# Performance work log

Hardware: AMD Instinct MI355X
Metric: run time of the kernel (lower is better)

The kernel has to match this reference:

```python
import jax, jax.numpy as jnp
import numpy as np

SCALES = (1, 3, 6)
PRECISION = 10  # pywt default: 2**10 samples of psi on [-5, 5]


def _gaus1_filters():
    """Replicates pywt.cwt's integrated-wavelet filters for wavelet='gaus1'.

    pywt: psi, x = wavelet.wavefun(10); int_psi = cumsum(psi)*step; per scale a:
    j = arange(a*(x[-1]-x[0])+1)/(a*step) -> int indices; filter = int_psi[j][::-1];
    conv = np.convolve(data, filter). np.convolve flips its kernel, so the
    equivalent cross-correlation kernel (lax.conv semantics) is int_psi[j].
    """
    x = np.linspace(-5.0, 5.0, 2 ** PRECISION)
    step = x[1] - x[0]
    psi = -2.0 * x * np.exp(-x ** 2) / (np.pi / 2.0) ** 0.25
    int_psi = np.cumsum(psi) * step
    filts = []
    for a in SCALES:
        j = (np.arange(a * (x[-1] - x[0]) + 1) / (a * step)).astype(np.int64)
        j = j[j < int_psi.size]
        filts.append(int_psi[j].astype(np.float32))  # correlation kernel
    return filts

_FILTS = _gaus1_filters()


def setup_inputs() -> dict:
    key = jax.random.key(0)
    x = jax.random.normal(key, (32, 4096, 64), dtype=jnp.float32)
    return {"x": x}


def reference(x):
    B, S, C = x.shape
    sig = jnp.transpose(x, (0, 2, 1)).reshape(B * C, 1, S)  # [B*C, 1, S]
    outs = []
    for a, f in zip(SCALES, _FILTS):
        L = f.shape[0]
        k = jnp.asarray(f).reshape(1, 1, L)
        # full convolution (np.convolve): pad L-1 both sides
        conv = jax.lax.conv_general_dilated(
            sig, k, window_strides=(1,), padding=[(L - 1, L - 1)],
            dimension_numbers=("NCH", "OIH", "NCH"))  # [B*C, 1, S+L-1]
        coef = -np.sqrt(a).astype(np.float32) * jnp.diff(conv, axis=-1)  # [B*C,1,S+L-2]
        d = (coef.shape[-1] - S) / 2.0
        coef = coef[..., int(np.floor(d)): coef.shape[-1] - int(np.ceil(d))]  # [B*C,1,S]
        outs.append(coef)
    out = jnp.concatenate(outs, axis=1).reshape(B, C, len(SCALES), S)
    return jnp.transpose(out, (0, 2, 3, 1))  # [B, 3, S, C]
```

## Files before the change

kernel.cpp:

```cpp
#include <hip/hip_runtime.h>
#include <math.h>

#define S_LEN  4096
#define NCH    64
#define TILE_S 64
#define NT     4
#define RPT    8
#define TY     8
#define NQR    48
#define NQS    49
#define WQ     18
#define PQ     5
#define WLEN   72

struct WtArgs { float w6[62]; float w3[32]; float w1[12]; };


template <int T, int R>
struct FmaR {
  static __device__ __forceinline__ void run(const WtArgs& W, const float (&win)[WLEN],
                                             float (&a6)[RPT], float (&a3)[RPT],
                                             float (&a1)[RPT]) {
    a6[R] = fmaf(W.w6[T], win[T + R + 1], a6[R]);
    if constexpr (T >= 15 && T <= 46) a3[R] = fmaf(W.w3[T - 15], win[T + R + 1], a3[R]);
    if constexpr (T >= 25 && T <= 36) a1[R] = fmaf(W.w1[T - 25], win[T + R + 1], a1[R]);
    FmaR<T, R + 1>::run(W, win, a6, a3, a1);
  }
};
template <int T>
struct FmaR<T, RPT> {
  static __device__ __forceinline__ void run(const WtArgs&, const float (&)[WLEN],
                                             float (&)[RPT], float (&)[RPT], float (&)[RPT]) {}
};

template <int Q>
static __device__ __forceinline__ void load_quad(const float* __restrict__ colbase, int Q0,
                                                 float (&win)[WLEN]) {
  int s = Q0 + Q; if (s >= NQR) s -= NQR;
  const float4 v = *(const float4*)(colbase + (s << 2));
  win[4 * Q + 0] = v.x; win[4 * Q + 1] = v.y; win[4 * Q + 2] = v.z; win[4 * Q + 3] = v.w;
}

template <int Q>
struct PreQ {
  static __device__ __forceinline__ void run(const float* __restrict__ colbase, int Q0,
                                             float (&win)[WLEN]) {
    load_quad<Q>(colbase, Q0, win);
    PreQ<Q + 1>::run(colbase, Q0, win);
  }
};
template <>
struct PreQ<PQ> {
  static __device__ __forceinline__ void run(const float* __restrict__, int, float (&)[WLEN]) {}
};

template <int T>
struct Step {
  static __device__ __forceinline__ void run(const float* __restrict__ colbase, int Q0,
                                             const WtArgs& W, float (&win)[WLEN],
                                             float (&a6)[RPT], float (&a3)[RPT],
                                             float (&a1)[RPT]) {
    if constexpr ((T % 4 == 0) && (T / 4 + PQ < WQ))
      load_quad<T / 4 + PQ>(colbase, Q0, win);
    FmaR<T, 0>::run(W, win, a6, a3, a1);
    Step<T + 1>::run(colbase, Q0, W, win, a6, a3, a1);
  }
};
template <>
struct Step<62> {
  static __device__ __forceinline__ void run(const float* __restrict__, int, const WtArgs&,
                                             float (&)[WLEN], float (&)[RPT],
                                             float (&)[RPT], float (&)[RPT]) {}
};

template <int R>
struct Store {
  static __device__ __forceinline__ void run(float* __restrict__ o1, float* __restrict__ o3,
                                             float* __restrict__ o6, const float (&a6)[RPT],
                                             const float (&a3)[RPT], const float (&a1)[RPT]) {
    o1[(size_t)R * NCH] = a1[R];
    o3[(size_t)R * NCH] = a3[R];
    o6[(size_t)R * NCH] = a6[R];
    Store<R + 1>::run(o1, o3, o6, a6, a3, a1);
  }
};
template <>
struct Store<RPT> {
  static __device__ __forceinline__ void run(float* __restrict__, float* __restrict__,
                                             float* __restrict__, const float (&)[RPT],
                                             const float (&)[RPT], const float (&)[RPT]) {}
};

template <int R>
struct Zero {
  static __device__ __forceinline__ void run(float (&a6)[RPT], float (&a3)[RPT], float (&a1)[RPT]) {
    a6[R] = 0.f; a3[R] = 0.f; a1[R] = 0.f;
    Zero<R + 1>::run(a6, a3, a1);
  }
};
template <>
struct Zero<RPT> {
  static __device__ __forceinline__ void run(float (&)[RPT], float (&)[RPT], float (&)[RPT]) {}
};

__global__ __launch_bounds__(512, 4)
void cwt_main(const float* __restrict__ x, float* __restrict__ out, const WtArgs W) {
  __shared__ __align__(16) float lds[NCH * NQS * 4];

  const int c  = threadIdx.x;
  const int ty = threadIdx.y;

  const int hw = blockIdx.x;
  const int wg = ((hw & 7) << 6) + (hw >> 3);
  const int gp = wg & 15;
  const int b  = wg >> 4;
  const int s0b = gp * (TILE_S * NT);
  const int ROW0 = s0b - 32;

  const float* __restrict__ xb = x + (size_t)b * S_LEN * NCH;
  const float* __restrict__ colbase = &lds[c * (NQS * 4)];

  {
    float pg[4][4];
    #pragma unroll
    for (int k = 0; k < 4; ++k) {
      const int g = 4 * ty + k;
      #pragma unroll
      for (int j = 0; j < 4; ++j) {
        const int row = ROW0 + 4 * g + j;
        float v = 0.f;
        if ((unsigned)row < (unsigned)S_LEN) v = xb[(size_t)row * NCH + c];
        pg[k][j] = v;
      }
    }
    #pragma unroll
    for (int k = 0; k < 4; ++k) {
      const int g = 4 * ty + k;
      *(float4*)&lds[c * (NQS * 4) + (g << 2)] =
          make_float4(pg[k][0], pg[k][1], pg[k][2], pg[k][3]);
    }
  }
  __syncthreads();

  #pragma clang loop unroll(disable)
  for (int i = 0; i < NT; ++i) {
    float sg[2][4];
    if (i < NT - 1) {
      #pragma unroll
      for (int k = 0; k < 2; ++k) {
        const int g = 32 + 16 * i + 2 * ty + k;
        #pragma unroll
        for (int j = 0; j < 4; ++j) {
          const int row = ROW0 + 4 * g + j;
          float v = 0.f;
          if ((unsigned)row < (unsigned)S_LEN) v = xb[(size_t)row * NCH + c];
          sg[k][j] = v;
        }
      }
    }

    float win[WLEN];
    float a6[RPT], a3[RPT], a1[RPT];
    Zero<0>::run(a6, a3, a1);
    const int Q0 = 16 * i + 2 * ty;
    PreQ<0>::run(colbase, Q0, win);
    Step<0>::run(colbase, Q0, W, win, a6, a3, a1);

    const int srow = s0b + TILE_S * i + RPT * ty;
    float* o1 = out + (((size_t)b * 3 + 0) * S_LEN + srow) * NCH + c;
    float* o3 = out + (((size_t)b * 3 + 1) * S_LEN + srow) * NCH + c;
    float* o6 = out + (((size_t)b * 3 + 2) * S_LEN + srow) * NCH + c;
    Store<0>::run(o1, o3, o6, a6, a3, a1);

    if (i < NT - 1) {
      #pragma unroll
      for (int k = 0; k < 2; ++k) {
        const int g = 32 + 16 * i + 2 * ty + k;
        const int s = (g < NQR) ? g : g - NQR;
        *(float4*)&lds[c * (NQS * 4) + (s << 2)] =
            make_float4(sg[k][0], sg[k][1], sg[k][2], sg[k][3]);
      }
    }
    __syncthreads();
  }
}

extern "C" void kernel_launch(void* const* d_in, const int* in_sizes, int n_in,
                              void* d_out, int out_size, void* d_ws, size_t ws_size,
                              hipStream_t stream) {
  (void)n_in; (void)out_size; (void)d_ws; (void)ws_size;
  const float* x = (const float*)d_in[0];
  float* out = (float*)d_out;
  const int B = in_sizes[0] / (S_LEN * NCH);

  WtArgs W;
  {
    static double ip[1024];
    const double delta = 10.0 / 1023.0;
    const double step  = (-5.0 + delta) + 5.0;
    const double cn    = pow(3.141592653589793 * 0.5, 0.25);
    double s = 0.0;
    for (int i = 0; i < 1024; ++i) {
      const double xi  = (i == 1023) ? 5.0 : ((double)i * delta - 5.0);
      const double psi = (-2.0 * xi) * exp(-(xi * xi)) / cn;
      s += psi;
      ip[i] = s * step;
    }
    const int   as_[3] = {6, 3, 1};
    const int   lf_[3] = {61, 31, 11};
    float*      wp_[3] = {W.w6, W.w3, W.w1};
    for (int si = 0; si < 3; ++si) {
      const double denom = (double)as_[si] * step;
      const float  sqa   = (float)sqrt((double)as_[si]);
      const int    lf    = lf_[si];
      for (int t = 0; t <= lf; ++t) {
        float km1 = 0.f, kt = 0.f;
        if (t >= 1)      km1 = (float)ip[(long)(((double)(t - 1)) / denom)];
        if (t <= lf - 1) kt  = (float)ip[(long)(((double)t) / denom)];
        wp_[si][t] = -sqa * (km1 - kt);
      }
    }
  }

  const int nblk = (S_LEN / (TILE_S * NT)) * B;
  dim3 grid(nblk);
  dim3 block(NCH, TY);
  hipLaunchKernelGGL(cwt_main, grid, block, 0, stream, x, out, W);
}
```

Measured before the change: 137.9 us.

## Bake filter weights as constexpr immediates and use one tile per block

```diff
diff --git a/kernel.cpp b/kernel.cpp
--- a/kernel.cpp
+++ b/kernel.cpp
@@ -4,49 +4,97 @@
 #define S_LEN  4096
 #define NCH    64
 #define TILE_S 64
-#define NT     4
 #define RPT    8
 #define TY     8
-#define NQR    48
-#define NQS    49
+#define NQ     32
+#define NQS    33
 #define WQ     18
 #define PQ     5
 #define WLEN   72
 
-struct WtArgs { float w6[62]; float w3[32]; float w1[12]; };
-
+
+constexpr double cexp_(double v) {
+  const double LN2 = 0.6931471805599453;
+  double t = v / LN2;
+  int k = (int)t;
+  if (t < 0.0 && (double)k != t) --k;
+  double r = v - (double)k * LN2;
+  double term = 1.0, sum = 1.0;
+  for (int n = 1; n <= 22; ++n) { term *= r / (double)n; sum += term; }
+  while (k > 0) { sum *= 2.0; --k; }
+  while (k < 0) { sum *= 0.5; ++k; }
+  return sum;
+}
+constexpr double csqrt_(double a) {
+  double y = a > 1.0 ? a : 1.0;
+  for (int i = 0; i < 64; ++i) y = 0.5 * (y + a / y);
+  return y;
+}
+struct Wt { float w6[62]; float w3[32]; float w1[12]; };
+constexpr Wt make_weights() {
+  Wt w{};
+  double ip[1024] = {};
+  const double delta = 10.0 / 1023.0;
+  const double step  = (-5.0 + delta) + 5.0;
+  const double cn    = csqrt_(csqrt_(1.5707963267948966));
+  double s = 0.0;
+  for (int i = 0; i < 1024; ++i) {
+    const double xi  = (i == 1023) ? 5.0 : ((double)i * delta - 5.0);
+    const double psi = (-2.0 * xi) * cexp_(-(xi * xi)) / cn;
+    s += psi;
+    ip[i] = s * step;
+  }
+  const int as_[3] = {6, 3, 1};
+  const int lf_[3] = {61, 31, 11};
+  for (int si = 0; si < 3; ++si) {
+    const double denom = (double)as_[si] * step;
+    const float  sqa   = (float)csqrt_((double)as_[si]);
+    const int    lf    = lf_[si];
+    for (int t = 0; t <= lf; ++t) {
+      float km1 = 0.f, kt = 0.f;
+      if (t >= 1)      km1 = (float)ip[(long)(((double)(t - 1)) / denom)];
+      if (t <= lf - 1) kt  = (float)ip[(long)(((double)t) / denom)];
+      const float val = -sqa * (km1 - kt);
+      if (si == 0) w.w6[t] = val; else if (si == 1) w.w3[t] = val; else w.w1[t] = val;
+    }
+  }
+  return w;
+}
+constexpr Wt CW = make_weights();
+template <int T> constexpr float W6 = CW.w6[T];
+template <int T> constexpr float W3 = CW.w3[T];
+template <int T> constexpr float W1 = CW.w1[T];
 
 template <int T, int R>
 struct FmaR {
-  static __device__ __forceinline__ void run(const WtArgs& W, const float (&win)[WLEN],
+  static __device__ __forceinline__ void run(const float (&win)[WLEN],
                                              float (&a6)[RPT], float (&a3)[RPT],
                                              float (&a1)[RPT]) {
-    a6[R] = fmaf(W.w6[T], win[T + R + 1], a6[R]);
-    if constexpr (T >= 15 && T <= 46) a3[R] = fmaf(W.w3[T - 15], win[T + R + 1], a3[R]);
-    if constexpr (T >= 25 && T <= 36) a1[R] = fmaf(W.w1[T - 25], win[T + R + 1], a1[R]);
-    FmaR<T, R + 1>::run(W, win, a6, a3, a1);
+    a6[R] = fmaf(W6<T>, win[T + R + 1], a6[R]);
+    if constexpr (T >= 15 && T <= 46) a3[R] = fmaf(W3<T - 15>, win[T + R + 1], a3[R]);
+    if constexpr (T >= 25 && T <= 36) a1[R] = fmaf(W1<T - 25>, win[T + R + 1], a1[R]);
+    FmaR<T, R + 1>::run(win, a6, a3, a1);
   }
 };
 template <int T>
 struct FmaR<T, RPT> {
-  static __device__ __forceinline__ void run(const WtArgs&, const float (&)[WLEN],
+  static __device__ __forceinline__ void run(const float (&)[WLEN],
                                              float (&)[RPT], float (&)[RPT], float (&)[RPT]) {}
 };
 
 template <int Q>
-static __device__ __forceinline__ void load_quad(const float* __restrict__ colbase, int Q0,
+static __device__ __forceinline__ void load_quad(const float* __restrict__ colbase, int q0,
                                                  float (&win)[WLEN]) {
-  int s = Q0 + Q; if (s >= NQR) s -= NQR;
-  const float4 v = *(const float4*)(colbase + (s << 2));
+  const float4 v = *(const float4*)(colbase + ((q0 + Q) << 2));
   win[4 * Q + 0] = v.x; win[4 * Q + 1] = v.y; win[4 * Q + 2] = v.z; win[4 * Q + 3] = v.w;
 }
 
 template <int Q>
 struct PreQ {
-  static __device__ __forceinline__ void run(const float* __restrict__ colbase, int Q0,
+  static __device__ __forceinline__ void run(const float* __restrict__ colbase, int q0,
                                              float (&win)[WLEN]) {
-    load_quad<Q>(colbase, Q0, win);
-    PreQ<Q + 1>::run(colbase, Q0, win);
+    load_quad<Q>(colbase, q0, win);
+    PreQ<Q + 1>::run(colbase, q0, win);
   }
 };
 template <>
@@ -56,21 +104,19 @@
 
 template <int T>
 struct Step {
-  static __device__ __forceinline__ void run(const float* __restrict__ colbase, int Q0,
-                                             const WtArgs& W, float (&win)[WLEN],
-                                             float (&a6)[RPT], float (&a3)[RPT],
-                                             float (&a1)[RPT]) {
+  static __device__ __forceinline__ void run(const float* __restrict__ colbase, int q0,
+                                             float (&win)[WLEN], float (&a6)[RPT],
+                                             float (&a3)[RPT], float (&a1)[RPT]) {
     if constexpr ((T % 4 == 0) && (T / 4 + PQ < WQ))
-      load_quad<T / 4 + PQ>(colbase, Q0, win);
-    FmaR<T, 0>::run(W, win, a6, a3, a1);
-    Step<T + 1>::run(colbase, Q0, W, win, a6, a3, a1);
+      load_quad<T / 4 + PQ>(colbase, q0, win);
+    FmaR<T, 0>::run(win, a6, a3, a1);
+    Step<T + 1>::run(colbase, q0, win, a6, a3, a1);
   }
 };
 template <>
 struct Step<62> {
-  static __device__ __forceinline__ void run(const float* __restrict__, int, const WtArgs&,
-                                             float (&)[WLEN], float (&)[RPT],
-                                             float (&)[RPT], float (&)[RPT]) {}
+  static __device__ __forceinline__ void run(const float* __restrict__, int, float (&)[WLEN],
+                                             float (&)[RPT], float (&)[RPT], float (&)[RPT]) {}
 };
 
 template <int R>
@@ -103,31 +149,29 @@
   static __device__ __forceinline__ void run(float (&)[RPT], float (&)[RPT], float (&)[RPT]) {}
 };
 
-__global__ __launch_bounds__(512, 4)
-void cwt_main(const float* __restrict__ x, float* __restrict__ out, const WtArgs W) {
+__global__ __launch_bounds__(512, 6)
+void cwt_main(const float* __restrict__ x, float* __restrict__ out) {
   __shared__ __align__(16) float lds[NCH * NQS * 4];
 
   const int c  = threadIdx.x;
   const int ty = threadIdx.y;
 
   const int hw = blockIdx.x;
-  const int wg = ((hw & 7) << 6) + (hw >> 3);
-  const int gp = wg & 15;
-  const int b  = wg >> 4;
-  const int s0b = gp * (TILE_S * NT);
-  const int ROW0 = s0b - 32;
+  const int wg = ((hw & 7) << 8) + (hw >> 3);
+  const int sx = wg & 63;
+  const int b  = wg >> 6;
+  const int s0 = sx * TILE_S;
+  const int ROW0 = s0 - 32;
 
   const float* __restrict__ xb = x + (size_t)b * S_LEN * NCH;
-  const float* __restrict__ colbase = &lds[c * (NQS * 4)];
 
   {
     float pg[4][4];
     #pragma unroll
     for (int k = 0; k < 4; ++k) {
-      const int g = 4 * ty + k;
       #pragma unroll
       for (int j = 0; j < 4; ++j) {
-        const int row = ROW0 + 4 * g + j;
+        const int row = ROW0 + 16 * ty + 4 * k + j;
         float v = 0.f;
         if ((unsigned)row < (unsigned)S_LEN) v = xb[(size_t)row * NCH + c];
         pg[k][j] = v;
@@ -135,54 +179,27 @@
     }
     #pragma unroll
     for (int k = 0; k < 4; ++k) {
-      const int g = 4 * ty + k;
-      *(float4*)&lds[c * (NQS * 4) + (g << 2)] =
+      const int q = 4 * ty + k;
+      *(float4*)&lds[c * (NQS * 4) + (q << 2)] =
           make_float4(pg[k][0], pg[k][1], pg[k][2], pg[k][3]);
     }
   }
   __syncthreads();
 
-  #pragma clang loop unroll(disable)
-  for (int i = 0; i < NT; ++i) {
-    float sg[2][4];
-    if (i < NT - 1) {
-      #pragma unroll
-      for (int k = 0; k < 2; ++k) {
-        const int g = 32 + 16 * i + 2 * ty + k;
-        #pragma unroll
-        for (int j = 0; j < 4; ++j) {
-          const int row = ROW0 + 4 * g + j;
-          float v = 0.f;
-          if ((unsigned)row < (unsigned)S_LEN) v = xb[(size_t)row * NCH + c];
-          sg[k][j] = v;
-        }
-      }
-    }
-
-    float win[WLEN];
-    float a6[RPT], a3[RPT], a1[RPT];
-    Zero<0>::run(a6, a3, a1);
-    const int Q0 = 16 * i + 2 * ty;
-    PreQ<0>::run(colbase, Q0, win);
-    Step<0>::run(colbase, Q0, W, win, a6, a3, a1);
-
-    const int srow = s0b + TILE_S * i + RPT * ty;
-    float* o1 = out + (((size_t)b * 3 + 0) * S_LEN + srow) * NCH + c;
-    float* o3 = out + (((size_t)b * 3 + 1) * S_LEN + srow) * NCH + c;
-    float* o6 = out + (((size_t)b * 3 + 2) * S_LEN + srow) * NCH + c;
-    Store<0>::run(o1, o3, o6, a6, a3, a1);
-
-    if (i < NT - 1) {
-      #pragma unroll
-      for (int k = 0; k < 2; ++k) {
-        const int g = 32 + 16 * i + 2 * ty + k;
-        const int s = (g < NQR) ? g : g - NQR;
-        *(float4*)&lds[c * (NQS * 4) + (s << 2)] =
-            make_float4(sg[k][0], sg[k][1], sg[k][2], sg[k][3]);
-      }
-    }
-    __syncthreads();
-  }
+  const float* __restrict__ colbase = &lds[c * (NQS * 4)];
+  const int q0 = 2 * ty;
+
+  float win[WLEN];
+  float a6[RPT], a3[RPT], a1[RPT];
+  Zero<0>::run(a6, a3, a1);
+  PreQ<0>::run(colbase, q0, win);
+  Step<0>::run(colbase, q0, win, a6, a3, a1);
+
+  const int srow = s0 + RPT * ty;
+  float* o1 = out + (((size_t)b * 3 + 0) * S_LEN + srow) * NCH + c;
+  float* o3 = out + (((size_t)b * 3 + 1) * S_LEN + srow) * NCH + c;
+  float* o6 = out + (((size_t)b * 3 + 2) * S_LEN + srow) * NCH + c;
+  Store<0>::run(o1, o3, o6, a6, a3, a1);
 }
 
 extern "C" void kernel_launch(void* const* d_in, const int* in_sizes, int n_in,
@@ -193,37 +210,8 @@
   float* out = (float*)d_out;
   const int B = in_sizes[0] / (S_LEN * NCH);
 
-  WtArgs W;
-  {
-    static double ip[1024];
-    const double delta = 10.0 / 1023.0;
-    const double step  = (-5.0 + delta) + 5.0;
-    const double cn    = pow(3.141592653589793 * 0.5, 0.25);
-    double s = 0.0;
-    for (int i = 0; i < 1024; ++i) {
-      const double xi  = (i == 1023) ? 5.0 : ((double)i * delta - 5.0);
-      const double psi = (-2.0 * xi) * exp(-(xi * xi)) / cn;
-      s += psi;
-      ip[i] = s * step;
-    }
-    const int   as_[3] = {6, 3, 1};
-    const int   lf_[3] = {61, 31, 11};
-    float*      wp_[3] = {W.w6, W.w3, W.w1};
-    for (int si = 0; si < 3; ++si) {
-      const double denom = (double)as_[si] * step;
-      const float  sqa   = (float)sqrt((double)as_[si]);
-      const int    lf    = lf_[si];
-      for (int t = 0; t <= lf; ++t) {
-        float km1 = 0.f, kt = 0.f;
-        if (t >= 1)      km1 = (float)ip[(long)(((double)(t - 1)) / denom)];
-        if (t <= lf - 1) kt  = (float)ip[(long)(((double)t) / denom)];
-        wp_[si][t] = -sqa * (km1 - kt);
-      }
-    }
-  }
-
-  const int nblk = (S_LEN / (TILE_S * NT)) * B;
+  const int nblk = (S_LEN / TILE_S) * B;
   dim3 grid(nblk);
   dim3 block(NCH, TY);
-  hipLaunchKernelGGL(cwt_main, grid, block, 0, stream, x, out, W);
-}
+  hipLaunchKernelGGL(cwt_main, grid, block, 0, stream, x, out);
+}
```

New measurement: 130.5 us. 5.4% less time.
